# Performance work log

Hardware: AMD Instinct MI355X
Metric: run time of the kernel (lower is better)

Reference implementation:

```python
import jax, jax.numpy as jnp
import numpy as np

B, N, D, H, E = 4, 1024, 512, 8, 5
HD = D // H  # head_dim = 64


def _xavier(k, shape):
    fan_out, fan_in = shape
    s = (2.0 / (fan_in + fan_out)) ** 0.5
    return jax.random.normal(k, shape, jnp.float32) * s


def setup_inputs() -> dict:
    key = jax.random.key(0)
    ks = jax.random.split(key, 7)
    x = jax.random.normal(ks[0], (B, N, D), jnp.float32)
    edge_features = jax.random.normal(ks[1], (B, N, N, E), jnp.float32)
    node_mask = jax.random.randint(ks[2], (B, N), 0, 2).astype(bool)
    w_qkv = _xavier(ks[3], (3 * D, D))
    w_ep = _xavier(ks[4], (H, E))
    w_eg = _xavier(ks[5], (H, E))
    b_eg = jnp.zeros((H,), jnp.float32)
    w_proj = _xavier(ks[6], (D, D))
    b_proj = jnp.zeros((D,), jnp.float32)
    return {"x": x, "edge_features": edge_features, "node_mask": node_mask,
            "w_qkv": w_qkv, "w_ep": w_ep, "w_eg": w_eg, "b_eg": b_eg,
            "w_proj": w_proj, "b_proj": b_proj}


def reference(x, edge_features, node_mask, w_qkv, w_ep, w_eg, b_eg, w_proj, b_proj):
    b, n, d = x.shape
    scale = HD ** -0.5
    # qkv projection (torch Linear: y = x @ W^T), split into q,k,v (b,H,n,HD)
    qkv = (x @ w_qkv.T).reshape(b, n, 3, H, HD)
    qkv = jnp.transpose(qkv, (2, 0, 3, 1, 4))
    q, k, v = qkv[0], qkv[1], qkv[2]
    # attention scores (b,H,n,n)
    scores = jnp.einsum('bhnd,bhmd->bhnm', q, k) * scale
    # edge bias and sigmoid gate, (b,n,n,E) @ (E,H) -> (b,H,n,n)
    edge_bias = jnp.einsum('bnme,he->bhnm', edge_features, w_ep)
    edge_gates = jax.nn.sigmoid(
        jnp.einsum('bnme,he->bhnm', edge_features, w_eg) + b_eg[None, :, None, None])
    scores = scores + edge_gates * edge_bias
    # pairwise valid mask, broadcast over heads
    m = node_mask[:, None, :, None] & node_mask[:, None, None, :]  # (b,1,n,n)
    scores = jnp.where(m, scores, -jnp.inf)
    row_valid = jnp.any(m, axis=-1)  # (b,1,n)
    scores = jnp.where(row_valid[..., None], scores, 0.0)
    attn = jax.nn.softmax(scores, axis=-1)
    out = jnp.einsum('bhnm,bhmd->bhnd', attn, v)
    out = jnp.transpose(out, (0, 2, 1, 3)).reshape(b, n, d)
    return out @ w_proj.T + b_proj
```

## Files before the change

kernel.cpp:

```cpp
#include <hip/hip_runtime.h>
#include <hip/hip_bf16.h>

#define Bb 4
#define Nn 1024
#define Dd 512
#define Hh 8
#define Ee 5
#define HDd 64

typedef unsigned int u32_t;
typedef unsigned short u16_t;
typedef short s16x8 __attribute__((ext_vector_type(8)));
typedef float f32x4 __attribute__((ext_vector_type(4)));

#define MFMA(a, b, c) __builtin_amdgcn_mfma_f32_16x16x32_bf16((a), (b), (c), 0, 0, 0)

__device__ __forceinline__ u32_t pack32(float x) {
    u32_t u = __float_as_uint(x);
    u32_t hi = u & 0xffff0000u;
    float rem = x - __uint_as_float(hi);
    u32_t r = __float_as_uint(rem);
    u32_t lo = (r + 0x7fffu + ((r >> 16) & 1u)) >> 16;
    return hi | (lo & 0xffffu);
}

__device__ __forceinline__ void unpk8(uint4 A, uint4 B, s16x8& h, s16x8& l) {
    union { u16_t u[8]; s16x8 v; } H, L;
    u32_t a[8] = {A.x, A.y, A.z, A.w, B.x, B.y, B.z, B.w};
    #pragma unroll
    for (int i = 0; i < 8; i++) { H.u[i] = (u16_t)(a[i] >> 16); L.u[i] = (u16_t)(a[i] & 0xffffu); }
    h = H.v; l = L.v;
}

__device__ __forceinline__ void split4(uint4 A, uint2& hi, uint2& lo) {
    hi.x = (A.x >> 16) | (A.y & 0xffff0000u);
    hi.y = (A.z >> 16) | (A.w & 0xffff0000u);
    lo.x = (A.x & 0xffffu) | (A.y << 16);
    lo.y = (A.z & 0xffffu) | (A.w << 16);
}

__device__ __forceinline__ void stage16(uint4 A0, uint4 A1, uint4 A2, uint4 A3,
                                        u16_t* dh, u16_t* dl) {
    uint2 h0, l0, h1, l1, h2, l2, h3, l3;
    split4(A0, h0, l0); split4(A1, h1, l1); split4(A2, h2, l2); split4(A3, h3, l3);
    *(uint4*)(dh + 0) = make_uint4(h0.x, h0.y, h1.x, h1.y);
    *(uint4*)(dh + 8) = make_uint4(h2.x, h2.y, h3.x, h3.y);
    *(uint4*)(dl + 0) = make_uint4(l0.x, l0.y, l1.x, l1.y);
    *(uint4*)(dl + 8) = make_uint4(l2.x, l2.y, l3.x, l3.y);
}

__global__ __launch_bounds__(256) void prep_mask(const void* __restrict__ msk,
                                                 int* __restrict__ mw,
                                                 int* __restrict__ anyB) {
    __shared__ int notint;
    __shared__ int ab[Bb];
    const int tid = threadIdx.x;
    if (tid == 0) notint = 0;
    if (tid < Bb) ab[tid] = 0;
    __syncthreads();
    const u32_t* wp = (const u32_t*)msk;
    int bad = 0;
    for (int i = tid; i < 1024; i += 256) bad |= (wp[i] > 1u);
    if (bad) atomicOr(&notint, 1);
    __syncthreads();
    const int isbyte = notint;
    const unsigned char* bp = (const unsigned char*)msk;
    for (int i = tid; i < Bb * Nn; i += 256) {
        const int v = isbyte ? (bp[i] != 0) : (wp[i] != 0);
        mw[i] = v;
        if (v) atomicOr(&ab[i >> 10], 1);
    }
    __syncthreads();
    if (tid < Bb) anyB[tid] = ab[tid];
}

__global__ __launch_bounds__(256) void pack3(const float* __restrict__ x,
                                             const float* __restrict__ wq,
                                             const float* __restrict__ wpj,
                                             u32_t* __restrict__ xp,
                                             u32_t* __restrict__ wqp,
                                             u32_t* __restrict__ wpp) {
    const int gt = blockIdx.x * 256 + threadIdx.x;
    const int gs = gridDim.x * 256;
    const float4* xs = (const float4*)x;
    uint4* xd = (uint4*)xp;
    for (int i = gt; i < (Bb * Nn * Dd) / 4; i += gs) {
        float4 v = xs[i];
        xd[i] = make_uint4(pack32(v.x), pack32(v.y), pack32(v.z), pack32(v.w));
    }
    const float4* qs = (const float4*)wq;
    uint4* qd = (uint4*)wqp;
    for (int i = gt; i < (3 * Dd * Dd) / 4; i += gs) {
        float4 v = qs[i];
        qd[i] = make_uint4(pack32(v.x), pack32(v.y), pack32(v.z), pack32(v.w));
    }
    const float4* ps = (const float4*)wpj;
    uint4* pd = (uint4*)wpp;
    for (int i = gt; i < (Dd * Dd) / 4; i += gs) {
        float4 v = ps[i];
        pd[i] = make_uint4(pack32(v.x), pack32(v.y), pack32(v.z), pack32(v.w));
    }
}

__global__ __launch_bounds__(256) void qkv_mfma(const u32_t* __restrict__ xp,
                                                const u32_t* __restrict__ wp,
                                                u32_t* __restrict__ q32,
                                                u32_t* __restrict__ k32,
                                                u32_t* __restrict__ v32) {
    __shared__ __align__(16) u16_t Xh[64 * 72], Xl[64 * 72];
    __shared__ __align__(16) u16_t Wh[64 * 72], Wl[64 * 72];
    const int tid = threadIdx.x;
    const int wv = tid >> 6, lane = tid & 63, lm = lane & 15, quad = lane >> 4;
    const int m0 = blockIdx.y * 64, c0 = blockIdx.x * 64;
    const int row = tid >> 2, dq = tid & 3;
    const uint4* x4 = (const uint4*)xp;
    const uint4* w4 = (const uint4*)wp;

    f32x4 acc[4];
    #pragma unroll
    for (int nt = 0; nt < 4; nt++) acc[nt] = {0.f, 0.f, 0.f, 0.f};

    for (int kt = 0; kt < 8; kt++) {
        __syncthreads();
        {
            const size_t xb = (size_t)(m0 + row) * 128 + kt * 16 + dq * 4;
            stage16(x4[xb + 0], x4[xb + 1], x4[xb + 2], x4[xb + 3],
                    &Xh[row * 72 + dq * 16], &Xl[row * 72 + dq * 16]);
            const size_t wb = (size_t)(c0 + row) * 128 + kt * 16 + dq * 4;
            stage16(w4[wb + 0], w4[wb + 1], w4[wb + 2], w4[wb + 3],
                    &Wh[row * 72 + dq * 16], &Wl[row * 72 + dq * 16]);
        }
        __syncthreads();
        s16x8 ah[2], al[2];
        #pragma unroll
        for (int ks = 0; ks < 2; ks++) {
            ah[ks] = *(const s16x8*)&Xh[(16 * wv + lm) * 72 + ks * 32 + quad * 8];
            al[ks] = *(const s16x8*)&Xl[(16 * wv + lm) * 72 + ks * 32 + quad * 8];
        }
        #pragma unroll
        for (int nt = 0; nt < 4; nt++) {
            #pragma unroll
            for (int ks = 0; ks < 2; ks++) {
                s16x8 bh = *(const s16x8*)&Wh[(16 * nt + lm) * 72 + ks * 32 + quad * 8];
                s16x8 bl = *(const s16x8*)&Wl[(16 * nt + lm) * 72 + ks * 32 + quad * 8];
                acc[nt] = MFMA(ah[ks], bh, acc[nt]);
                acc[nt] = MFMA(ah[ks], bl, acc[nt]);
                acc[nt] = MFMA(al[ks], bh, acc[nt]);
            }
        }
    }
    #pragma unroll
    for (int nt = 0; nt < 4; nt++) {
        const int c = c0 + 16 * nt + lm;
        const int s = c >> 9, hd = c & 511, h = hd >> 6, d = hd & 63;
        u32_t* dst = (s == 0) ? q32 : (s == 1) ? k32 : v32;
        #pragma unroll
        for (int r = 0; r < 4; r++) {
            const int m = m0 + 16 * wv + 4 * quad + r;
            const int b = m >> 10, n = m & (Nn - 1);
            dst[(((size_t)b * Hh + h) * Nn + n) * HDd + d] = pack32(acc[nt][r]);
        }
    }
}

__global__ __launch_bounds__(256, 2) void attn_mfma(const u32_t* __restrict__ q32,
                                                    const u32_t* __restrict__ k32,
                                                    const u32_t* __restrict__ v32,
                                                    const float* __restrict__ ef,
                                                    const int* __restrict__ mw,
                                                    const int* __restrict__ anyB,
                                                    const float* __restrict__ wep,
                                                    const float* __restrict__ weg,
                                                    const float* __restrict__ beg,
                                                    u32_t* __restrict__ aoutp) {
    __shared__ __align__(16) u16_t Qh[64 * 72], Ql[64 * 72];
    __shared__ __align__(16) u16_t Kh[64 * 72], Kl[64 * 72];
    __shared__ __align__(16) u16_t VTh[64 * 88], VTl[64 * 88];
    __shared__ __align__(16) u32_t Ppk[64 * 68];

    const int tid = threadIdx.x;
    const int wv = tid >> 6, lane = tid & 63, lm = lane & 15, quad = lane >> 4;
    const int i0 = blockIdx.x * 64;
    const int h  = blockIdx.y;
    const int b  = blockIdx.z;

    const float wp0 = wep[h*Ee+0], wp1 = wep[h*Ee+1], wp2 = wep[h*Ee+2],
                wp3 = wep[h*Ee+3], wp4 = wep[h*Ee+4];
    const float wg0 = weg[h*Ee+0], wg1 = weg[h*Ee+1], wg2 = weg[h*Ee+2],
                wg3 = weg[h*Ee+3], wg4 = weg[h*Ee+4];
    const float bgs = beg[h];

    const uint4* qg4 = (const uint4*)(q32 + (((size_t)b * Hh + h) * Nn + i0) * HDd);
    const uint4* kg4 = (const uint4*)(k32 + (((size_t)b * Hh + h) * Nn) * HDd);
    const uint4* vg4 = (const uint4*)(v32 + (((size_t)b * Hh + h) * Nn) * HDd);
    const int* mwB = mw + b * Nn;

    {
        const int row = tid >> 2, dq = tid & 3;
        const size_t qb = (size_t)row * 16 + dq * 4;
        stage16(qg4[qb + 0], qg4[qb + 1], qg4[qb + 2], qg4[qb + 3],
                &Qh[row * 72 + dq * 16], &Ql[row * 72 + dq * 16]);
    }
    __syncthreads();
    s16x8 qh[2], ql[2];
    #pragma unroll
    for (int ks = 0; ks < 2; ks++) {
        qh[ks] = *(const s16x8*)&Qh[(16 * wv + lm) * 72 + ks * 32 + quad * 8];
        ql[ks] = *(const s16x8*)&Ql[(16 * wv + lm) * 72 + ks * 32 + quad * 8];
    }

    const int anyb = anyB[b];
    const int i_sm = i0 + 16 * wv + lm;
    const int rvs = anyb && mwB[i_sm];
    float m_ = -1e30f, l_ = 0.f;
    f32x4 accO[4];
    #pragma unroll
    for (int dn = 0; dn < 4; dn++) accO[dn] = {0.f, 0.f, 0.f, 0.f};
    const float* efL = ef + ((size_t)(b * Nn + i_sm) * Nn + 4 * quad) * Ee;
    const int xk = 8 * (lm & 3);

    for (int jt = 0; jt < Nn / 64; jt++) {
        const int j0 = jt * 64;

        int4 mj4[4];
        float4 er4[4][5];
        #pragma unroll
        for (int jn = 0; jn < 4; jn++) {
            mj4[jn] = *(const int4*)&mwB[j0 + 16 * jn + 4 * quad];
            const float4* p4 = (const float4*)(efL + (size_t)(j0 + 16 * jn) * Ee);
            #pragma unroll
            for (int c = 0; c < 5; c++) er4[jn][c] = p4[c];
        }

        __syncthreads();

        {
            const int row = tid >> 2, dq = tid & 3;
            const size_t kb = (size_t)(j0 + row) * 16 + dq * 4;
            stage16(kg4[kb + 0], kg4[kb + 1], kg4[kb + 2], kg4[kb + 3],
                    &Kh[row * 72 + dq * 16], &Kl[row * 72 + dq * 16]);
        }
        {
            const int jg = tid & 15, dc = tid >> 4;
            u32_t r0[4], r1[4], r2[4], r3[4];
            uint4 A0 = vg4[(j0 + 4 * jg + 0) * 16 + dc];
            uint4 A1 = vg4[(j0 + 4 * jg + 1) * 16 + dc];
            uint4 A2 = vg4[(j0 + 4 * jg + 2) * 16 + dc];
            uint4 A3 = vg4[(j0 + 4 * jg + 3) * 16 + dc];
            r0[0]=A0.x; r0[1]=A0.y; r0[2]=A0.z; r0[3]=A0.w;
            r1[0]=A1.x; r1[1]=A1.y; r1[2]=A1.z; r1[3]=A1.w;
            r2[0]=A2.x; r2[1]=A2.y; r2[2]=A2.z; r2[3]=A2.w;
            r3[0]=A3.x; r3[1]=A3.y; r3[2]=A3.z; r3[3]=A3.w;
            #pragma unroll
            for (int c = 0; c < 4; c++) {
                const int d = 4 * dc + c;
                uint2 hi, lo;
                hi.x = (r0[c] >> 16) | (r1[c] & 0xffff0000u);
                hi.y = (r2[c] >> 16) | (r3[c] & 0xffff0000u);
                lo.x = (r0[c] & 0xffffu) | (r1[c] << 16);
                lo.y = (r2[c] & 0xffffu) | (r3[c] << 16);
                *(uint2*)&VTh[d * 88 + 4 * jg] = hi;
                *(uint2*)&VTl[d * 88 + 4 * jg] = lo;
            }
        }
        __syncthreads();

        f32x4 Sp[4];
        #pragma unroll
        for (int jn = 0; jn < 4; jn++) {
            f32x4 s = {0.f, 0.f, 0.f, 0.f};
            #pragma unroll
            for (int ks = 0; ks < 2; ks++) {
                s16x8 kh = *(const s16x8*)&Kh[(16 * jn + lm) * 72 + ks * 32 + quad * 8];
                s16x8 kl = *(const s16x8*)&Kl[(16 * jn + lm) * 72 + ks * 32 + quad * 8];
                s = MFMA(kh, qh[ks], s);
                s = MFMA(kh, ql[ks], s);
                s = MFMA(kl, qh[ks], s);
            }
            Sp[jn] = s;
        }

        float pp[4][4];
        #pragma unroll
        for (int jn = 0; jn < 4; jn++) {
            const int mjv[4] = {mj4[jn].x, mj4[jn].y, mj4[jn].z, mj4[jn].w};
            #pragma unroll
            for (int r = 0; r < 4; r++) {
                const int f = r * 5;
                const float e0 = er4[jn][(f+0)>>2][(f+0)&3];
                const float e1 = er4[jn][(f+1)>>2][(f+1)&3];
                const float e2 = er4[jn][(f+2)>>2][(f+2)&3];
                const float e3 = er4[jn][(f+3)>>2][(f+3)&3];
                const float e4 = er4[jn][(f+4)>>2][(f+4)&3];
                const float bias = fmaf(e0, wp0, fmaf(e1, wp1, fmaf(e2, wp2, fmaf(e3, wp3, e4 * wp4))));
                const float gv = fmaf(e0, wg0, fmaf(e1, wg1, fmaf(e2, wg2, fmaf(e3, wg3, fmaf(e4, wg4, bgs)))));
                const float gate = __builtin_amdgcn_rcpf(1.f + __expf(-gv));
                const float val = fmaf(Sp[jn][r], 0.125f, gate * bias);
                pp[jn][r] = rvs ? (mjv[r] ? val : -1e30f) : 0.f;
            }
        }
        float tmax = fmaxf(fmaxf(fmaxf(pp[0][0], pp[0][1]), fmaxf(pp[0][2], pp[0][3])),
                           fmaxf(fmaxf(pp[1][0], pp[1][1]), fmaxf(pp[1][2], pp[1][3])));
        tmax = fmaxf(tmax,
               fmaxf(fmaxf(fmaxf(pp[2][0], pp[2][1]), fmaxf(pp[2][2], pp[2][3])),
                     fmaxf(fmaxf(pp[3][0], pp[3][1]), fmaxf(pp[3][2], pp[3][3]))));
        tmax = fmaxf(tmax, __shfl_xor(tmax, 16));
        tmax = fmaxf(tmax, __shfl_xor(tmax, 32));
        const float mnew = fmaxf(m_, tmax);
        const float alpha = __expf(m_ - mnew);
        float ps = 0.f;
        #pragma unroll
        for (int jn = 0; jn < 4; jn++)
            #pragma unroll
            for (int r = 0; r < 4; r++) { pp[jn][r] = __expf(pp[jn][r] - mnew); ps += pp[jn][r]; }
        ps += __shfl_xor(ps, 16);
        ps += __shfl_xor(ps, 32);
        m_ = mnew;
        l_ = l_ * alpha + ps;
        float a4[4];
        #pragma unroll
        for (int r = 0; r < 4; r++) a4[r] = __shfl(alpha, 4 * quad + r);
        #pragma unroll
        for (int dn = 0; dn < 4; dn++)
            #pragma unroll
            for (int r = 0; r < 4; r++) accO[dn][r] *= a4[r];

        #pragma unroll
        for (int jn = 0; jn < 4; jn++) {
            #pragma unroll
            for (int p = 0; p < 2; p++) {
                const int col = (16 * jn + 4 * quad + 2 * p) ^ xk;
                *(uint2*)&Ppk[(16 * wv + lm) * 68 + col] =
                    make_uint2(pack32(pp[jn][2 * p]), pack32(pp[jn][2 * p + 1]));
            }
        }

        s16x8 ph[2], pl[2];
        #pragma unroll
        for (int ks2 = 0; ks2 < 2; ks2++) {
            const int off = (16 * wv + lm) * 68 + ((ks2 * 32 + quad * 8) ^ xk);
            uint4 A = *(const uint4*)&Ppk[off];
            uint4 B2 = *(const uint4*)&Ppk[off + 4];
            unpk8(A, B2, ph[ks2], pl[ks2]);
        }
        #pragma unroll
        for (int dn = 0; dn < 4; dn++) {
            f32x4 c = accO[dn];
            #pragma unroll
            for (int ks2 = 0; ks2 < 2; ks2++) {
                s16x8 vh = *(const s16x8*)&VTh[(16 * dn + lm) * 88 + ks2 * 32 + quad * 8];
                s16x8 vl = *(const s16x8*)&VTl[(16 * dn + lm) * 88 + ks2 * 32 + quad * 8];
                c = MFMA(ph[ks2], vh, c);
                c = MFMA(ph[ks2], vl, c);
                c = MFMA(pl[ks2], vh, c);
            }
            accO[dn] = c;
        }
    }

    float linv[4];
    #pragma unroll
    for (int r = 0; r < 4; r++) linv[r] = __builtin_amdgcn_rcpf(__shfl(l_, 4 * quad + r));
    #pragma unroll
    for (int r = 0; r < 4; r++) {
        const int i = i0 + 16 * wv + 4 * quad + r;
        #pragma unroll
        for (int dn = 0; dn < 4; dn++)
            aoutp[(size_t)(b * Nn + i) * Dd + h * HDd + 16 * dn + lm] = pack32(accO[dn][r] * linv[r]);
    }
}

__global__ __launch_bounds__(256) void out_mfma(const u32_t* __restrict__ ap,
                                                const u32_t* __restrict__ wp,
                                                const float* __restrict__ bias,
                                                float* __restrict__ out) {
    __shared__ __align__(16) u16_t Xh[64 * 72], Xl[64 * 72];
    __shared__ __align__(16) u16_t Wh[64 * 72], Wl[64 * 72];
    const int tid = threadIdx.x;
    const int wv = tid >> 6, lane = tid & 63, lm = lane & 15, quad = lane >> 4;
    const int m0 = blockIdx.y * 64, c0 = blockIdx.x * 64;
    const int row = tid >> 2, dq = tid & 3;
    const uint4* a4 = (const uint4*)ap;
    const uint4* w4 = (const uint4*)wp;

    f32x4 acc[4];
    #pragma unroll
    for (int nt = 0; nt < 4; nt++) acc[nt] = {0.f, 0.f, 0.f, 0.f};

    for (int kt = 0; kt < 8; kt++) {
        __syncthreads();
        {
            const size_t ab = (size_t)(m0 + row) * 128 + kt * 16 + dq * 4;
            stage16(a4[ab + 0], a4[ab + 1], a4[ab + 2], a4[ab + 3],
                    &Xh[row * 72 + dq * 16], &Xl[row * 72 + dq * 16]);
            const size_t wb = (size_t)(c0 + row) * 128 + kt * 16 + dq * 4;
            stage16(w4[wb + 0], w4[wb + 1], w4[wb + 2], w4[wb + 3],
                    &Wh[row * 72 + dq * 16], &Wl[row * 72 + dq * 16]);
        }
        __syncthreads();
        s16x8 ah[2], al[2];
        #pragma unroll
        for (int ks = 0; ks < 2; ks++) {
            ah[ks] = *(const s16x8*)&Xh[(16 * wv + lm) * 72 + ks * 32 + quad * 8];
            al[ks] = *(const s16x8*)&Xl[(16 * wv + lm) * 72 + ks * 32 + quad * 8];
        }
        #pragma unroll
        for (int nt = 0; nt < 4; nt++) {
            #pragma unroll
            for (int ks = 0; ks < 2; ks++) {
                s16x8 bh = *(const s16x8*)&Wh[(16 * nt + lm) * 72 + ks * 32 + quad * 8];
                s16x8 bl = *(const s16x8*)&Wl[(16 * nt + lm) * 72 + ks * 32 + quad * 8];
                acc[nt] = MFMA(ah[ks], bh, acc[nt]);
                acc[nt] = MFMA(ah[ks], bl, acc[nt]);
                acc[nt] = MFMA(al[ks], bh, acc[nt]);
            }
        }
    }
    #pragma unroll
    for (int nt = 0; nt < 4; nt++) {
        const int c = c0 + 16 * nt + lm;
        const float bc = bias[c];
        #pragma unroll
        for (int r = 0; r < 4; r++) {
            const int m = m0 + 16 * wv + 4 * quad + r;
            out[(size_t)m * Dd + c] = acc[nt][r] + bc;
        }
    }
}

extern "C" void kernel_launch(void* const* d_in, const int* in_sizes, int n_in,
                              void* d_out, int out_size, void* d_ws, size_t ws_size,
                              hipStream_t stream) {
    const float* x    = (const float*)d_in[0];
    const float* ef   = (const float*)d_in[1];
    const void*  msk  = d_in[2];
    const float* wqkv = (const float*)d_in[3];
    const float* wep  = (const float*)d_in[4];
    const float* weg  = (const float*)d_in[5];
    const float* beg  = (const float*)d_in[6];
    const float* wpj  = (const float*)d_in[7];
    const float* bpj  = (const float*)d_in[8];
    float* out = (float*)d_out;

    int* mw   = (int*)d_ws;
    int* anyB = mw + Bb * Nn;
    u32_t* q32 = (u32_t*)(anyB + 16);
    const size_t per = (size_t)Bb * Hh * Nn * HDd;
    u32_t* k32 = q32 + per;
    u32_t* v32 = k32 + per;
    u32_t* aop = v32 + per;
    u32_t* xp  = aop + (size_t)Bb * Nn * Dd;
    u32_t* wqp = xp + (size_t)Bb * Nn * Dd;
    u32_t* wpp = wqp + (size_t)3 * Dd * Dd;

    prep_mask<<<1, 256, 0, stream>>>(msk, mw, anyB);
    pack3<<<1024, 256, 0, stream>>>(x, wqkv, wpj, xp, wqp, wpp);
    qkv_mfma<<<dim3(24, 64), 256, 0, stream>>>(xp, wqp, q32, k32, v32);
    attn_mfma<<<dim3(Nn / 64, Hh, Bb), 256, 0, stream>>>(q32, k32, v32, ef, mw, anyB,
                                                         wep, weg, beg, aop);
    out_mfma<<<dim3(8, 64), 256, 0, stream>>>(aop, wpp, bpj, out);
}
```

Before: 335.2 us.

## Register-prefetch next tiles in GEMM and attention kernels, merge prep kernels

Each GEMM and the attention loop now load the next K-tile (and next K/V/edge-feature/mask tile) into registers before computing the current one. This overlaps global-memory latency with MFMA and softmax work. Plain __syncthreads is replaced with an LDS-wait plus s_barrier helper. The mask-prep and packing kernels are merged into one launch using an extra block. The trade-off is higher register pressure, which may reduce occupancy.

```diff
diff --git a/kernel.cpp b/kernel.cpp
--- a/kernel.cpp
+++ b/kernel.cpp
@@ -14,6 +14,12 @@
 typedef float f32x4 __attribute__((ext_vector_type(4)));
 
 #define MFMA(a, b, c) __builtin_amdgcn_mfma_f32_16x16x32_bf16((a), (b), (c), 0, 0, 0)
+
+__device__ __forceinline__ void lds_barrier() {
+    asm volatile("s_waitcnt lgkmcnt(0)" ::: "memory");
+    __builtin_amdgcn_s_barrier();
+    asm volatile("" ::: "memory");
+}
 
 __device__ __forceinline__ u32_t pack32(float x) {
     u32_t u = __float_as_uint(x);
@@ -49,39 +55,40 @@
     *(uint4*)(dl + 8) = make_uint4(l2.x, l2.y, l3.x, l3.y);
 }
 
-__global__ __launch_bounds__(256) void prep_mask(const void* __restrict__ msk,
+__global__ __launch_bounds__(256) void pack_prep(const float* __restrict__ x,
+                                                 const float* __restrict__ wq,
+                                                 const float* __restrict__ wpj,
+                                                 const void* __restrict__ msk,
+                                                 u32_t* __restrict__ xp,
+                                                 u32_t* __restrict__ wqp,
+                                                 u32_t* __restrict__ wpp,
                                                  int* __restrict__ mw,
                                                  int* __restrict__ anyB) {
     __shared__ int notint;
     __shared__ int ab[Bb];
     const int tid = threadIdx.x;
-    if (tid == 0) notint = 0;
-    if (tid < Bb) ab[tid] = 0;
-    __syncthreads();
-    const u32_t* wp = (const u32_t*)msk;
-    int bad = 0;
-    for (int i = tid; i < 1024; i += 256) bad |= (wp[i] > 1u);
-    if (bad) atomicOr(&notint, 1);
-    __syncthreads();
-    const int isbyte = notint;
-    const unsigned char* bp = (const unsigned char*)msk;
-    for (int i = tid; i < Bb * Nn; i += 256) {
-        const int v = isbyte ? (bp[i] != 0) : (wp[i] != 0);
-        mw[i] = v;
-        if (v) atomicOr(&ab[i >> 10], 1);
-    }
-    __syncthreads();
-    if (tid < Bb) anyB[tid] = ab[tid];
-}
-
-__global__ __launch_bounds__(256) void pack3(const float* __restrict__ x,
-                                             const float* __restrict__ wq,
-                                             const float* __restrict__ wpj,
-                                             u32_t* __restrict__ xp,
-                                             u32_t* __restrict__ wqp,
-                                             u32_t* __restrict__ wpp) {
-    const int gt = blockIdx.x * 256 + threadIdx.x;
-    const int gs = gridDim.x * 256;
+    if (blockIdx.x == 1024) {
+        if (tid == 0) notint = 0;
+        if (tid < Bb) ab[tid] = 0;
+        __syncthreads();
+        const u32_t* wp = (const u32_t*)msk;
+        int bad = 0;
+        for (int i = tid; i < 1024; i += 256) bad |= (wp[i] > 1u);
+        if (bad) atomicOr(&notint, 1);
+        __syncthreads();
+        const int isbyte = notint;
+        const unsigned char* bp = (const unsigned char*)msk;
+        for (int i = tid; i < Bb * Nn; i += 256) {
+            const int v = isbyte ? (bp[i] != 0) : (wp[i] != 0);
+            mw[i] = v;
+            if (v) atomicOr(&ab[i >> 10], 1);
+        }
+        __syncthreads();
+        if (tid < Bb) anyB[tid] = ab[tid];
+        return;
+    }
+    const int gt = blockIdx.x * 256 + tid;
+    const int gs = 1024 * 256;
     const float4* xs = (const float4*)x;
     uint4* xd = (uint4*)xp;
     for (int i = gt; i < (Bb * Nn * Dd) / 4; i += gs) {
@@ -116,21 +123,25 @@
     const uint4* x4 = (const uint4*)xp;
     const uint4* w4 = (const uint4*)wp;
 
+    const size_t xb0 = (size_t)(m0 + row) * 128 + dq * 4;
+    const size_t wb0 = (size_t)(c0 + row) * 128 + dq * 4;
+    uint4 xa0 = x4[xb0 + 0], xa1 = x4[xb0 + 1], xa2 = x4[xb0 + 2], xa3 = x4[xb0 + 3];
+    uint4 wa0 = w4[wb0 + 0], wa1 = w4[wb0 + 1], wa2 = w4[wb0 + 2], wa3 = w4[wb0 + 3];
+
     f32x4 acc[4];
     #pragma unroll
     for (int nt = 0; nt < 4; nt++) acc[nt] = {0.f, 0.f, 0.f, 0.f};
 
     for (int kt = 0; kt < 8; kt++) {
-        __syncthreads();
-        {
-            const size_t xb = (size_t)(m0 + row) * 128 + kt * 16 + dq * 4;
-            stage16(x4[xb + 0], x4[xb + 1], x4[xb + 2], x4[xb + 3],
-                    &Xh[row * 72 + dq * 16], &Xl[row * 72 + dq * 16]);
-            const size_t wb = (size_t)(c0 + row) * 128 + kt * 16 + dq * 4;
-            stage16(w4[wb + 0], w4[wb + 1], w4[wb + 2], w4[wb + 3],
-                    &Wh[row * 72 + dq * 16], &Wl[row * 72 + dq * 16]);
-        }
-        __syncthreads();
+        lds_barrier();
+        stage16(xa0, xa1, xa2, xa3, &Xh[row * 72 + dq * 16], &Xl[row * 72 + dq * 16]);
+        stage16(wa0, wa1, wa2, wa3, &Wh[row * 72 + dq * 16], &Wl[row * 72 + dq * 16]);
+        const int ktn = (kt < 7) ? kt + 1 : 7;
+        xa0 = x4[xb0 + ktn * 16 + 0]; xa1 = x4[xb0 + ktn * 16 + 1];
+        xa2 = x4[xb0 + ktn * 16 + 2]; xa3 = x4[xb0 + ktn * 16 + 3];
+        wa0 = w4[wb0 + ktn * 16 + 0]; wa1 = w4[wb0 + ktn * 16 + 1];
+        wa2 = w4[wb0 + ktn * 16 + 2]; wa3 = w4[wb0 + ktn * 16 + 3];
+        lds_barrier();
         s16x8 ah[2], al[2];
         #pragma unroll
         for (int ks = 0; ks < 2; ks++) {
@@ -183,25 +194,42 @@
     const int i0 = blockIdx.x * 64;
     const int h  = blockIdx.y;
     const int b  = blockIdx.z;
+    const int row = tid >> 2, dq = tid & 3;
+    const int jg = tid >> 4, dc = tid & 15;
+
+    const uint4* qg4 = (const uint4*)(q32 + (((size_t)b * Hh + h) * Nn + i0) * HDd);
+    const uint4* kg4 = (const uint4*)(k32 + (((size_t)b * Hh + h) * Nn) * HDd);
+    const uint4* vg4 = (const uint4*)(v32 + (((size_t)b * Hh + h) * Nn) * HDd);
+    const int* mwB = mw + b * Nn;
+
+    const size_t qb = (size_t)row * 16 + dq * 4;
+    uint4 qA0 = qg4[qb + 0], qA1 = qg4[qb + 1], qA2 = qg4[qb + 2], qA3 = qg4[qb + 3];
+    uint4 kr0 = kg4[qb + 0], kr1 = kg4[qb + 1], kr2 = kg4[qb + 2], kr3 = kg4[qb + 3];
+    uint4 vr0 = vg4[(4 * jg + 0) * 16 + dc], vr1 = vg4[(4 * jg + 1) * 16 + dc],
+          vr2 = vg4[(4 * jg + 2) * 16 + dc], vr3 = vg4[(4 * jg + 3) * 16 + dc];
+
+    const int i_sm = i0 + 16 * wv + lm;
+    const float* efL = ef + ((size_t)(b * Nn + i_sm) * Nn + 4 * quad) * Ee;
+    int4 mj4[4];
+    float4 er4[4][5];
+    #pragma unroll
+    for (int jn = 0; jn < 4; jn++) {
+        mj4[jn] = *(const int4*)&mwB[16 * jn + 4 * quad];
+        const float4* p4 = (const float4*)(efL + (size_t)(16 * jn) * Ee);
+        #pragma unroll
+        for (int c = 0; c < 5; c++) er4[jn][c] = p4[c];
+    }
 
     const float wp0 = wep[h*Ee+0], wp1 = wep[h*Ee+1], wp2 = wep[h*Ee+2],
                 wp3 = wep[h*Ee+3], wp4 = wep[h*Ee+4];
     const float wg0 = weg[h*Ee+0], wg1 = weg[h*Ee+1], wg2 = weg[h*Ee+2],
                 wg3 = weg[h*Ee+3], wg4 = weg[h*Ee+4];
     const float bgs = beg[h];
-
-    const uint4* qg4 = (const uint4*)(q32 + (((size_t)b * Hh + h) * Nn + i0) * HDd);
-    const uint4* kg4 = (const uint4*)(k32 + (((size_t)b * Hh + h) * Nn) * HDd);
-    const uint4* vg4 = (const uint4*)(v32 + (((size_t)b * Hh + h) * Nn) * HDd);
-    const int* mwB = mw + b * Nn;
-
-    {
-        const int row = tid >> 2, dq = tid & 3;
-        const size_t qb = (size_t)row * 16 + dq * 4;
-        stage16(qg4[qb + 0], qg4[qb + 1], qg4[qb + 2], qg4[qb + 3],
-                &Qh[row * 72 + dq * 16], &Ql[row * 72 + dq * 16]);
-    }
-    __syncthreads();
+    const int anyb = anyB[b];
+    const int rvs = anyb && mwB[i_sm];
+
+    stage16(qA0, qA1, qA2, qA3, &Qh[row * 72 + dq * 16], &Ql[row * 72 + dq * 16]);
+    lds_barrier();
     s16x8 qh[2], ql[2];
     #pragma unroll
     for (int ks = 0; ks < 2; ks++) {
@@ -209,48 +237,24 @@
         ql[ks] = *(const s16x8*)&Ql[(16 * wv + lm) * 72 + ks * 32 + quad * 8];
     }
 
-    const int anyb = anyB[b];
-    const int i_sm = i0 + 16 * wv + lm;
-    const int rvs = anyb && mwB[i_sm];
     float m_ = -1e30f, l_ = 0.f;
     f32x4 accO[4];
     #pragma unroll
     for (int dn = 0; dn < 4; dn++) accO[dn] = {0.f, 0.f, 0.f, 0.f};
-    const float* efL = ef + ((size_t)(b * Nn + i_sm) * Nn + 4 * quad) * Ee;
     const int xk = 8 * (lm & 3);
 
     for (int jt = 0; jt < Nn / 64; jt++) {
-        const int j0 = jt * 64;
-
-        int4 mj4[4];
-        float4 er4[4][5];
-        #pragma unroll
-        for (int jn = 0; jn < 4; jn++) {
-            mj4[jn] = *(const int4*)&mwB[j0 + 16 * jn + 4 * quad];
-            const float4* p4 = (const float4*)(efL + (size_t)(j0 + 16 * jn) * Ee);
-            #pragma unroll
-            for (int c = 0; c < 5; c++) er4[jn][c] = p4[c];
-        }
-
-        __syncthreads();
-
+        const int jtn = (jt + 1 < Nn / 64) ? jt + 1 : Nn / 64 - 1;
+        const int j0n = jtn * 64;
+
+        lds_barrier();
+
+        stage16(kr0, kr1, kr2, kr3, &Kh[row * 72 + dq * 16], &Kl[row * 72 + dq * 16]);
         {
-            const int row = tid >> 2, dq = tid & 3;
-            const size_t kb = (size_t)(j0 + row) * 16 + dq * 4;
-            stage16(kg4[kb + 0], kg4[kb + 1], kg4[kb + 2], kg4[kb + 3],
-                    &Kh[row * 72 + dq * 16], &Kl[row * 72 + dq * 16]);
-        }
-        {
-            const int jg = tid & 15, dc = tid >> 4;
-            u32_t r0[4], r1[4], r2[4], r3[4];
-            uint4 A0 = vg4[(j0 + 4 * jg + 0) * 16 + dc];
-            uint4 A1 = vg4[(j0 + 4 * jg + 1) * 16 + dc];
-            uint4 A2 = vg4[(j0 + 4 * jg + 2) * 16 + dc];
-            uint4 A3 = vg4[(j0 + 4 * jg + 3) * 16 + dc];
-            r0[0]=A0.x; r0[1]=A0.y; r0[2]=A0.z; r0[3]=A0.w;
-            r1[0]=A1.x; r1[1]=A1.y; r1[2]=A1.z; r1[3]=A1.w;
-            r2[0]=A2.x; r2[1]=A2.y; r2[2]=A2.z; r2[3]=A2.w;
-            r3[0]=A3.x; r3[1]=A3.y; r3[2]=A3.z; r3[3]=A3.w;
+            u32_t r0[4] = {vr0.x, vr0.y, vr0.z, vr0.w};
+            u32_t r1[4] = {vr1.x, vr1.y, vr1.z, vr1.w};
+            u32_t r2[4] = {vr2.x, vr2.y, vr2.z, vr2.w};
+            u32_t r3[4] = {vr3.x, vr3.y, vr3.z, vr3.w};
             #pragma unroll
             for (int c = 0; c < 4; c++) {
                 const int d = 4 * dc + c;
@@ -263,7 +267,16 @@
                 *(uint2*)&VTl[d * 88 + 4 * jg] = lo;
             }
         }
-        __syncthreads();
+        {
+            const size_t kbn = (size_t)(j0n + row) * 16 + dq * 4;
+            kr0 = kg4[kbn + 0]; kr1 = kg4[kbn + 1]; kr2 = kg4[kbn + 2]; kr3 = kg4[kbn + 3];
+            vr0 = vg4[(j0n + 4 * jg + 0) * 16 + dc];
+            vr1 = vg4[(j0n + 4 * jg + 1) * 16 + dc];
+            vr2 = vg4[(j0n + 4 * jg + 2) * 16 + dc];
+            vr3 = vg4[(j0n + 4 * jg + 3) * 16 + dc];
+        }
+
+        lds_barrier();
 
         f32x4 Sp[4];
         #pragma unroll
@@ -299,6 +312,14 @@
                 pp[jn][r] = rvs ? (mjv[r] ? val : -1e30f) : 0.f;
             }
         }
+        #pragma unroll
+        for (int jn = 0; jn < 4; jn++) {
+            mj4[jn] = *(const int4*)&mwB[j0n + 16 * jn + 4 * quad];
+            const float4* p4 = (const float4*)(efL + (size_t)(j0n + 16 * jn) * Ee);
+            #pragma unroll
+            for (int c = 0; c < 5; c++) er4[jn][c] = p4[c];
+        }
+
         float tmax = fmaxf(fmaxf(fmaxf(pp[0][0], pp[0][1]), fmaxf(pp[0][2], pp[0][3])),
                            fmaxf(fmaxf(pp[1][0], pp[1][1]), fmaxf(pp[1][2], pp[1][3])));
         tmax = fmaxf(tmax,
@@ -383,21 +404,25 @@
     const uint4* a4 = (const uint4*)ap;
     const uint4* w4 = (const uint4*)wp;
 
+    const size_t ab0 = (size_t)(m0 + row) * 128 + dq * 4;
+    const size_t wb0 = (size_t)(c0 + row) * 128 + dq * 4;
+    uint4 xa0 = a4[ab0 + 0], xa1 = a4[ab0 + 1], xa2 = a4[ab0 + 2], xa3 = a4[ab0 + 3];
+    uint4 wa0 = w4[wb0 + 0], wa1 = w4[wb0 + 1], wa2 = w4[wb0 + 2], wa3 = w4[wb0 + 3];
+
     f32x4 acc[4];
     #pragma unroll
     for (int nt = 0; nt < 4; nt++) acc[nt] = {0.f, 0.f, 0.f, 0.f};
 
     for (int kt = 0; kt < 8; kt++) {
-        __syncthreads();
-        {
-            const size_t ab = (size_t)(m0 + row) * 128 + kt * 16 + dq * 4;
-            stage16(a4[ab + 0], a4[ab + 1], a4[ab + 2], a4[ab + 3],
-                    &Xh[row * 72 + dq * 16], &Xl[row * 72 + dq * 16]);
-            const size_t wb = (size_t)(c0 + row) * 128 + kt * 16 + dq * 4;
-            stage16(w4[wb + 0], w4[wb + 1], w4[wb + 2], w4[wb + 3],
-                    &Wh[row * 72 + dq * 16], &Wl[row * 72 + dq * 16]);
-        }
-        __syncthreads();
+        lds_barrier();
+        stage16(xa0, xa1, xa2, xa3, &Xh[row * 72 + dq * 16], &Xl[row * 72 + dq * 16]);
+        stage16(wa0, wa1, wa2, wa3, &Wh[row * 72 + dq * 16], &Wl[row * 72 + dq * 16]);
+        const int ktn = (kt < 7) ? kt + 1 : 7;
+        xa0 = a4[ab0 + ktn * 16 + 0]; xa1 = a4[ab0 + ktn * 16 + 1];
+        xa2 = a4[ab0 + ktn * 16 + 2]; xa3 = a4[ab0 + ktn * 16 + 3];
+        wa0 = w4[wb0 + ktn * 16 + 0]; wa1 = w4[wb0 + ktn * 16 + 1];
+        wa2 = w4[wb0 + ktn * 16 + 2]; wa3 = w4[wb0 + ktn * 16 + 3];
+        lds_barrier();
         s16x8 ah[2], al[2];
         #pragma unroll
         for (int ks = 0; ks < 2; ks++) {
@@ -453,8 +478,7 @@
     u32_t* wqp = xp + (size_t)Bb * Nn * Dd;
     u32_t* wpp = wqp + (size_t)3 * Dd * Dd;
 
-    prep_mask<<<1, 256, 0, stream>>>(msk, mw, anyB);
-    pack3<<<1024, 256, 0, stream>>>(x, wqkv, wpj, xp, wqp, wpp);
+    pack_prep<<<1025, 256, 0, stream>>>(x, wqkv, wpj, msk, xp, wqp, wpp, mw, anyB);
     qkv_mfma<<<dim3(24, 64), 256, 0, stream>>>(xp, wqp, q32, k32, v32);
     attn_mfma<<<dim3(Nn / 64, Hh, Bb), 256, 0, stream>>>(q32, k32, v32, ef, mw, anyB,
                                                          wep, weg, beg, aop);
```

New measurement: 310.8 us. 1.08x faster.
